# Performance work log

Hardware: AMD Instinct MI355X
Metric: run time of the kernel (lower is better)

## Reference

```python
import jax, jax.numpy as jnp
import numpy as np

B = 8          # batch
K = 200        # tex_params (PCA components)
N_UV = 5023    # number of uv query points (FLAME vertex count)
V = 786432     # 512*512*3 flat texture size


def setup_inputs() -> dict:
    key = jax.random.key(0)
    k1, k2, k3, k4 = jax.random.split(key, 4)
    texcode = jax.random.normal(k1, (B, K), dtype=jnp.float32)
    uv_coords = jax.random.uniform(k2, (N_UV, 2), dtype=jnp.float32)
    texture_mean = jax.random.normal(k3, (1, 1, V), dtype=jnp.float32)
    texture_basis = jax.random.normal(k4, (1, V, K), dtype=jnp.float32) * 0.01
    return {
        "texcode": texcode,
        "uv_coords": uv_coords,
        "texture_mean": texture_mean,
        "texture_basis": texture_basis,
    }


def reference(texcode, uv_coords, texture_mean, texture_basis):
    # PCA linear combination: mean + basis @ texcode  (expressed as GEMM, not
    # a materialized (B, V, K) elementwise product)
    tex = texture_mean[0] + jnp.einsum("vk,bk->bv", texture_basis[0], texcode)  # (B, V)
    tex = tex.reshape(B, 512, 512, 3).transpose(0, 3, 1, 2)  # (B, 3, 512, 512)
    # F.interpolate(size=[256,256]) defaults to nearest: src index = floor(i*512/256) = 2i
    tex = tex[:, :, ::2, ::2]  # (B, 3, 256, 256)
    tex = tex[:, ::-1, :, :]   # channel reorder [2, 1, 0] (RGB -> BGR)
    x = jnp.clip((uv_coords[:, 0] * 256.0).astype(jnp.int32), 0, 255)
    y = jnp.clip(((1.0 - uv_coords[:, 1]) * 256.0).astype(jnp.int32), 0, 255)
    return tex[:, :, y, x]  # (B, 3, N_UV)
```

## Files before the change

kernel.cpp:

```cpp
#include <hip/hip_runtime.h>


#define B_SZ 8
#define K_SZ 200
#define PAIRS_PER_BLOCK 4

__global__ __launch_bounds__(256) void flametex_sample_kernel(
    const float* __restrict__ texcode,
    const float* __restrict__ uv,
    const float* __restrict__ mean,
    const float* __restrict__ basis,
    float* __restrict__ out,
    int N)
{
    __shared__ float s_tex[B_SZ * K_SZ];

    const int tid = threadIdx.x;

    for (int i = tid; i < B_SZ * K_SZ; i += 256)
        s_tex[i] = texcode[i];
    __syncthreads();

    const int p = blockIdx.x * PAIRS_PER_BLOCK + (tid >> 6);
    if (p >= 3 * N) return;

    const int n = p / 3;
    const int c = p - 3 * n;

    const int lane = tid & 63;
    const int kg   = lane >> 3;
    const int b    = lane & 7;

    const float u0 = uv[2 * n + 0];
    const float u1 = uv[2 * n + 1];
    int xi = (int)(u0 * 256.0f);
    xi = min(max(xi, 0), 255);
    int yi = (int)((1.0f - u1) * 256.0f);
    yi = min(max(yi, 0), 255);
    const int v = 3072 * yi + 6 * xi + (2 - c);

    const float* __restrict__ brow = basis + (long long)v * K_SZ + kg * 25;
    const float* __restrict__ trow = s_tex + b * K_SZ + kg * 25;

    float acc = 0.0f;
#pragma unroll
    for (int i = 0; i < 25; ++i)
        acc += brow[i] * trow[i];

    acc += __shfl_xor(acc, 8, 64);
    acc += __shfl_xor(acc, 16, 64);
    acc += __shfl_xor(acc, 32, 64);

    if (kg == 0)
        out[((long long)b * 3 + c) * N + n] = mean[v] + acc;
}

extern "C" void kernel_launch(void* const* d_in, const int* in_sizes, int n_in,
                              void* d_out, int out_size, void* d_ws, size_t ws_size,
                              hipStream_t stream) {
    const float* texcode = (const float*)d_in[0];
    const float* uv      = (const float*)d_in[1];
    const float* mean    = (const float*)d_in[2];
    const float* basis   = (const float*)d_in[3];
    float* out = (float*)d_out;

    const int N = in_sizes[1] / 2;
    const int total = 3 * N;
    const int blocks = (total + PAIRS_PER_BLOCK - 1) / PAIRS_PER_BLOCK;

    flametex_sample_kernel<<<blocks, 256, 0, stream>>>(texcode, uv, mean, basis, out, N);
}
```

Before: 673.9 us.

## Drop shared-memory texcode staging and use interleaved float4 basis loads

Removes the per-block copy of texcode into shared memory and the barrier that follows it, and reads texcode directly from global memory (cached in L1/L2). The basis row is split across the 8 k-groups in an interleaved float4 pattern, so that adjacent lanes read contiguous 16-byte chunks instead of strided 25-float slices, with a scalar tail for the last 8 elements. The uv pair is read as a single float2, and the mean load is hoisted before the dot product so its latency overlaps with it. This relies on the basis rows and texcode being 16-byte aligned (200 floats per row satisfies this), and it increases global and cache traffic for texcode.

```diff
diff --git a/kernel.cpp b/kernel.cpp
--- a/kernel.cpp
+++ b/kernel.cpp
@@ -1,7 +1,6 @@
 #include <hip/hip_runtime.h>
 
 
-#define B_SZ 8
 #define K_SZ 200
 #define PAIRS_PER_BLOCK 4
 
@@ -13,14 +12,7 @@
     float* __restrict__ out,
     int N)
 {
-    __shared__ float s_tex[B_SZ * K_SZ];
-
     const int tid = threadIdx.x;
-
-    for (int i = tid; i < B_SZ * K_SZ; i += 256)
-        s_tex[i] = texcode[i];
-    __syncthreads();
-
     const int p = blockIdx.x * PAIRS_PER_BLOCK + (tid >> 6);
     if (p >= 3 * N) return;
 
@@ -31,28 +23,38 @@
     const int kg   = lane >> 3;
     const int b    = lane & 7;
 
-    const float u0 = uv[2 * n + 0];
-    const float u1 = uv[2 * n + 1];
-    int xi = (int)(u0 * 256.0f);
+    const float2 uvn = reinterpret_cast<const float2*>(uv)[n];
+    int xi = (int)(uvn.x * 256.0f);
     xi = min(max(xi, 0), 255);
-    int yi = (int)((1.0f - u1) * 256.0f);
+    int yi = (int)((1.0f - uvn.y) * 256.0f);
     yi = min(max(yi, 0), 255);
     const int v = 3072 * yi + 6 * xi + (2 - c);
 
-    const float* __restrict__ brow = basis + (long long)v * K_SZ + kg * 25;
-    const float* __restrict__ trow = s_tex + b * K_SZ + kg * 25;
+    const float mv = mean[v];
+
+    const float4* __restrict__ b4 =
+        reinterpret_cast<const float4*>(basis + (long long)v * K_SZ) + kg;
+    const float4* __restrict__ t4 =
+        reinterpret_cast<const float4*>(texcode + b * K_SZ) + kg;
 
     float acc = 0.0f;
 #pragma unroll
-    for (int i = 0; i < 25; ++i)
-        acc += brow[i] * trow[i];
+    for (int i = 0; i < 6; ++i) {
+        const float4 bb = b4[i * 8];
+        const float4 tt = t4[i * 8];
+        acc += bb.x * tt.x;
+        acc += bb.y * tt.y;
+        acc += bb.z * tt.z;
+        acc += bb.w * tt.w;
+    }
+    acc += basis[(long long)v * K_SZ + 192 + kg] * texcode[b * K_SZ + 192 + kg];
 
     acc += __shfl_xor(acc, 8, 64);
     acc += __shfl_xor(acc, 16, 64);
     acc += __shfl_xor(acc, 32, 64);
 
     if (kg == 0)
-        out[((long long)b * 3 + c) * N + n] = mean[v] + acc;
+        out[((long long)b * 3 + c) * N + n] = mv + acc;
 }
 
 extern "C" void kernel_launch(void* const* d_in, const int* in_sizes, int n_in,
```

Measured after the change: 672.0 us. No clear change (-0.3%).
